# Performance work log

Measured on AMD Instinct MI355X. Metric: run time of the kernel, lower is better.

## Reference

```python
import jax, jax.numpy as jnp
import numpy as np

RADIUS = 0.5
HEADS = 4
LATENT = 128
KIN = 3 + 3 + 3 + 1  # q_pos + o_pos + rel + dist
LN_EPS = 1e-5


def setup_inputs() -> dict:
    key = jax.random.key(0)
    ks = jax.random.split(key, 12)
    B, Nq, No = 2, 1024, 1024
    h_obs = jax.random.normal(ks[0], (B, No, LATENT), dtype=jnp.float32)
    pos_obs = jax.random.uniform(ks[1], (B, No, 3), dtype=jnp.float32)
    pos_query = jax.random.uniform(ks[2], (B, Nq, 3), dtype=jnp.float32)
    obs_mask = jax.random.randint(ks[3], (B, No), 0, 2, dtype=jnp.int32)
    # kernel MLP params: Linear(KIN, LATENT) -> ReLU -> Linear(LATENT, HEADS)
    W1 = jax.random.normal(ks[4], (KIN, LATENT), dtype=jnp.float32) * (1.0 / np.sqrt(KIN))
    b1 = jax.random.normal(ks[5], (LATENT,), dtype=jnp.float32) * 0.01
    W2 = jax.random.normal(ks[6], (LATENT, HEADS), dtype=jnp.float32) * (1.0 / np.sqrt(LATENT))
    b2 = jax.random.normal(ks[7], (HEADS,), dtype=jnp.float32) * 0.01
    ln_g = jnp.ones((LATENT,), dtype=jnp.float32)
    ln_b = jnp.zeros((LATENT,), dtype=jnp.float32)
    Wv = jax.random.normal(ks[8], (LATENT, LATENT), dtype=jnp.float32) * (1.0 / np.sqrt(LATENT))
    bv = jax.random.normal(ks[9], (LATENT,), dtype=jnp.float32) * 0.01
    return {"h_obs": h_obs, "pos_obs": pos_obs, "pos_query": pos_query,
            "obs_mask": obs_mask, "W1": W1, "b1": b1, "W2": W2, "b2": b2,
            "ln_g": ln_g, "ln_b": ln_b, "Wv": Wv, "bv": bv}


def reference(h_obs, pos_obs, pos_query, obs_mask, W1, b1, W2, b2, ln_g, ln_b, Wv, bv):
    B, Nq, _ = pos_query.shape
    _, No, _ = pos_obs.shape
    H, D = HEADS, LATENT // HEADS

    # pairwise geometric encoding: (B, Nq, No, *)
    rel = pos_query[:, :, None, :] - pos_obs[:, None, :, :]
    dist = jnp.linalg.norm(rel, axis=-1, keepdims=True)
    q_exp = jnp.broadcast_to(pos_query[:, :, None, :], rel.shape)
    o_exp = jnp.broadcast_to(pos_obs[:, None, :, :], rel.shape)
    kin = jnp.concatenate([q_exp, o_exp, rel, dist], axis=-1)  # (B,Nq,No,KIN)

    # per-pair MLP -> per-head attention logits
    hid = jax.nn.relu(kin @ W1 + b1)                 # (B,Nq,No,LATENT)
    logits = hid @ W2 + b2                           # (B,Nq,No,H)
    logits = jnp.transpose(logits, (0, 3, 1, 2))     # (B,H,Nq,No)

    # radius + observation masking
    neg = jnp.float32(-jnp.inf)
    mask = (dist[..., 0] > RADIUS)[:, None, :, :] | (obs_mask == 0)[:, None, None, :]
    logits = jnp.where(mask, neg, logits)
    weights = jax.nn.softmax(logits, axis=-1)        # (B,H,Nq,No)

    # value path: LayerNorm + projection
    mu = jnp.mean(h_obs, axis=-1, keepdims=True)
    var = jnp.var(h_obs, axis=-1, keepdims=True)
    hn = (h_obs - mu) / jnp.sqrt(var + LN_EPS) * ln_g + ln_b
    v = hn @ Wv + bv                                 # (B,No,LATENT)
    v = jnp.transpose(v.reshape(B, No, H, D), (0, 2, 1, 3))  # (B,H,No,D)

    out = jnp.einsum('bhqo,bhod->bhqd', weights, v)  # (B,H,Nq,D)
    out = jnp.transpose(out, (0, 2, 1, 3)).reshape(B, Nq, H * D)
    return out
```

## Files before the change

kernel.cpp:

```cpp
#include <hip/hip_runtime.h>
#include <math.h>
#include <float.h>

#define B_ 2
#define NQ 1024
#define NO 1024
#define LAT 128
#define NHEADS 4
#define RADIUS_ 0.5f
#define LN_EPS_ 1e-5f
#define PW_STRIDE 68

#define V_BYTES ((size_t)B_ * NO * LAT * 4)

__device__ __forceinline__ float selh(int h, float a, float b, float c, float d) {
  return h == 0 ? a : (h == 1 ? b : (h == 2 ? c : d));
}

__global__ __launch_bounds__(256) void gano_prep_kernel(
    const float* __restrict__ h_obs, const float* __restrict__ ln_g,
    const float* __restrict__ ln_b, const float* __restrict__ Wv,
    const float* __restrict__ bv, float* __restrict__ v_out)
{
  const int tid = threadIdx.x;
  const int j = tid & 127;
  const int half = tid >> 7;
  const int wave = tid >> 6;
  const int lane = tid & 63;
  const int r0 = blockIdx.x * 4 + half * 2;

  __shared__ float s_redA[2][4];
  __shared__ float s_redB[2][4];
  __shared__ __align__(16) float s_hn[4][LAT];

  const float x0 = h_obs[(size_t)r0 * LAT + j];
  const float x1 = h_obs[(size_t)(r0 + 1) * LAT + j];
  float s0 = x0, s1 = x1;
  #pragma unroll
  for (int off = 32; off >= 1; off >>= 1) {
    s0 += __shfl_down(s0, off);
    s1 += __shfl_down(s1, off);
  }
  if (lane == 0) { s_redA[0][wave] = s0; s_redA[1][wave] = s1; }
  __syncthreads();
  const float mu0 = (s_redA[0][half * 2] + s_redA[0][half * 2 + 1]) * (1.0f / LAT);
  const float mu1 = (s_redA[1][half * 2] + s_redA[1][half * 2 + 1]) * (1.0f / LAT);
  const float d0 = x0 - mu0, d1 = x1 - mu1;
  float q0 = d0 * d0, q1 = d1 * d1;
  #pragma unroll
  for (int off = 32; off >= 1; off >>= 1) {
    q0 += __shfl_down(q0, off);
    q1 += __shfl_down(q1, off);
  }
  if (lane == 0) { s_redB[0][wave] = q0; s_redB[1][wave] = q1; }
  __syncthreads();
  const float var0 = (s_redB[0][half * 2] + s_redB[0][half * 2 + 1]) * (1.0f / LAT);
  const float var1 = (s_redB[1][half * 2] + s_redB[1][half * 2 + 1]) * (1.0f / LAT);
  const float g = ln_g[j], be = ln_b[j];
  s_hn[half * 2 + 0][j] = d0 * rsqrtf(var0 + LN_EPS_) * g + be;
  s_hn[half * 2 + 1][j] = d1 * rsqrtf(var1 + LN_EPS_) * g + be;
  __syncthreads();

  float a0 = 0.0f, a1 = 0.0f;
  const float4* h0 = (const float4*)s_hn[half * 2 + 0];
  const float4* h1 = (const float4*)s_hn[half * 2 + 1];
  #pragma unroll 4
  for (int k4 = 0; k4 < LAT / 4; ++k4) {
    const float4 u0 = h0[k4];
    const float4 u1 = h1[k4];
    const float w0 = Wv[(k4 * 4 + 0) * LAT + j];
    const float w1 = Wv[(k4 * 4 + 1) * LAT + j];
    const float w2 = Wv[(k4 * 4 + 2) * LAT + j];
    const float w3 = Wv[(k4 * 4 + 3) * LAT + j];
    a0 = fmaf(u0.x, w0, a0); a0 = fmaf(u0.y, w1, a0);
    a0 = fmaf(u0.z, w2, a0); a0 = fmaf(u0.w, w3, a0);
    a1 = fmaf(u1.x, w0, a1); a1 = fmaf(u1.y, w1, a1);
    a1 = fmaf(u1.z, w2, a1); a1 = fmaf(u1.w, w3, a1);
  }
  const float bvj = bv[j];
  v_out[(size_t)(r0 + 0) * LAT + j] = a0 + bvj;
  v_out[(size_t)(r0 + 1) * LAT + j] = a1 + bvj;
}

__global__ __launch_bounds__(256, 6) void gano_main_kernel(
    const float* __restrict__ pos_obs, const float* __restrict__ pos_query,
    const int* __restrict__ obs_mask,
    const float* __restrict__ W1, const float* __restrict__ b1,
    const float* __restrict__ W2, const float* __restrict__ b2,
    const float* __restrict__ v, float* __restrict__ out)
{
  __shared__ int   s_vidx[NO];
  __shared__ float s_vdist[NO];
  __shared__ __align__(16) float s_w[LAT][8];
  __shared__ __align__(16) float s_Q[LAT];
  __shared__ __align__(16) float s_pw[4][NHEADS][PW_STRIDE];
  __shared__ float s_mz[4][2][NHEADS];
  __shared__ int   s_cnt[16];

  const int tid = threadIdx.x;
  const int wave = tid >> 6, lane = tid & 63;
  const int bid = blockIdx.x;
  const int b = bid >> 10, q = bid & (NQ - 1);

  const float qx = pos_query[((size_t)b * NQ + q) * 3 + 0];
  const float qy = pos_query[((size_t)b * NQ + q) * 3 + 1];
  const float qz = pos_query[((size_t)b * NQ + q) * 3 + 2];

  if (tid < LAT) {
    const int j = tid;
    float w[10];
    #pragma unroll
    for (int k = 0; k < 10; ++k) w[k] = W1[k * LAT + j];
    s_w[j][0] = w[3] - w[6];
    s_w[j][1] = w[4] - w[7];
    s_w[j][2] = w[5] - w[8];
    s_w[j][3] = w[9];
    const float4 w2r = *(const float4*)&W2[j * NHEADS];
    s_w[j][4] = w2r.x; s_w[j][5] = w2r.y; s_w[j][6] = w2r.z; s_w[j][7] = w2r.w;
    s_Q[j] = b1[j] + qx * (w[0] + w[6]) + qy * (w[1] + w[7]) + qz * (w[2] + w[8]);
  }

  const float* pob = pos_obs + (size_t)b * NO * 3;
  const int*   om  = obs_mask + (size_t)b * NO;
  float dists[4];
  unsigned long long bals[4];
  #pragma unroll
  for (int rd = 0; rd < 4; ++rd) {
    const int o = (rd << 8) + tid;
    const float ox = pob[o * 3 + 0], oy = pob[o * 3 + 1], oz = pob[o * 3 + 2];
    const float rx = qx - ox, ry = qy - oy, rz = qz - oz;
    const float dist = sqrtf(rx * rx + ry * ry + rz * rz);
    const int ok = (om[o] != 0) && (dist <= RADIUS_);
    const unsigned long long bal = __ballot(ok);
    if (lane == 0) s_cnt[(rd << 2) + wave] = __popcll(bal);
    bals[rd] = bal;
    dists[rd] = dist;
  }
  __syncthreads();
  int Nv = 0;
  #pragma unroll
  for (int k = 0; k < 16; ++k) Nv += s_cnt[k];
  #pragma unroll
  for (int rd = 0; rd < 4; ++rd) {
    const int slot = (rd << 2) + wave;
    int base = 0;
    for (int k = 0; k < slot; ++k) base += s_cnt[k];
    if ((bals[rd] >> lane) & 1ull) {
      const int pos = base + __popcll(bals[rd] & ((1ull << lane) - 1ull));
      s_vidx[pos] = (rd << 8) + tid;
      s_vdist[pos] = dists[rd];
    }
  }
  __syncthreads();

  const int c0 = lane << 1;
  const int hh = lane >> 4;
  const float* vbl = v + (size_t)b * NO * LAT + c0;
  const float b20 = b2[0], b21 = b2[1], b22 = b2[2], b23 = b2[3];

  float m0 = -FLT_MAX, m1 = -FLT_MAX, m2 = -FLT_MAX, m3 = -FLT_MAX;
  float z0 = 0.f, z1 = 0.f, z2 = 0.f, z3 = 0.f;
  float ax = 0.f, ay = 0.f;

  for (int cbase = wave << 6; cbase < Nv; cbase += 256) {
    const int cnt = min(64, Nv - cbase);
    const bool act = lane < cnt;
    const int slot = cbase + (act ? lane : (cnt - 1));
    const int idx = s_vidx[slot];
    const float dist = s_vdist[slot];
    const float ox = pob[idx * 3 + 0], oy = pob[idx * 3 + 1], oz = pob[idx * 3 + 2];

    float a0 = b20, a1 = b21, a2 = b22, a3 = b23;
    #pragma unroll 2
    for (int j4 = 0; j4 < LAT / 4; ++j4) {
      const float4 q4 = *(const float4*)&s_Q[j4 << 2];
      #pragma unroll
      for (int u = 0; u < 4; ++u) {
        const int j = (j4 << 2) + u;
        const float4 cw = *(const float4*)&s_w[j][0];
        const float4 w2 = *(const float4*)&s_w[j][4];
        const float qj = (u == 0) ? q4.x : (u == 1) ? q4.y : (u == 2) ? q4.z : q4.w;
        float gg = fmaf(cw.x, ox, qj);
        gg = fmaf(cw.y, oy, gg);
        gg = fmaf(cw.z, oz, gg);
        gg = fmaf(cw.w, dist, gg);
        gg = fmaxf(gg, 0.0f);
        a0 = fmaf(gg, w2.x, a0);
        a1 = fmaf(gg, w2.y, a1);
        a2 = fmaf(gg, w2.z, a2);
        a3 = fmaf(gg, w2.w, a3);
      }
    }
    const float l0 = act ? a0 : -FLT_MAX;
    const float l1 = act ? a1 : -FLT_MAX;
    const float l2 = act ? a2 : -FLT_MAX;
    const float l3 = act ? a3 : -FLT_MAX;

    float x0 = l0, x1 = l1, x2 = l2, x3 = l3;
    #pragma unroll
    for (int off = 1; off < 64; off <<= 1) {
      x0 = fmaxf(x0, __shfl_xor(x0, off));
      x1 = fmaxf(x1, __shfl_xor(x1, off));
      x2 = fmaxf(x2, __shfl_xor(x2, off));
      x3 = fmaxf(x3, __shfl_xor(x3, off));
    }
    const float nm0 = fmaxf(m0, x0), nm1 = fmaxf(m1, x1);
    const float nm2 = fmaxf(m2, x2), nm3 = fmaxf(m3, x3);
    const float sc0 = __expf(m0 - nm0), sc1 = __expf(m1 - nm1);
    const float sc2 = __expf(m2 - nm2), sc3 = __expf(m3 - nm3);
    m0 = nm0; m1 = nm1; m2 = nm2; m3 = nm3;

    const float p0 = __expf(l0 - nm0);
    const float p1 = __expf(l1 - nm1);
    const float p2 = __expf(l2 - nm2);
    const float p3 = __expf(l3 - nm3);
    s_pw[wave][0][lane] = p0;
    s_pw[wave][1][lane] = p1;
    s_pw[wave][2][lane] = p2;
    s_pw[wave][3][lane] = p3;
    z0 = z0 * sc0 + p0;
    z1 = z1 * sc1 + p1;
    z2 = z2 * sc2 + p2;
    z3 = z3 * sc3 + p3;
    const float sch = selh(hh, sc0, sc1, sc2, sc3);
    ax *= sch; ay *= sch;

    const float* pr = s_pw[wave][hh];
    for (int it = 0; it < cnt; it += 4) {
      const float4 pq = *(const float4*)&pr[it];
      const int4 iq = *(const int4*)&s_vidx[cbase + it];
      const int i0 = iq.x & (NO - 1), i1 = iq.y & (NO - 1);
      const int i2 = iq.z & (NO - 1), i3 = iq.w & (NO - 1);
      const float2 v0 = *(const float2*)(vbl + (size_t)i0 * LAT);
      const float2 v1 = *(const float2*)(vbl + (size_t)i1 * LAT);
      const float2 v2 = *(const float2*)(vbl + (size_t)i2 * LAT);
      const float2 v3 = *(const float2*)(vbl + (size_t)i3 * LAT);
      ax = fmaf(pq.x, v0.x, ax); ay = fmaf(pq.x, v0.y, ay);
      ax = fmaf(pq.y, v1.x, ax); ay = fmaf(pq.y, v1.y, ay);
      ax = fmaf(pq.z, v2.x, ax); ay = fmaf(pq.z, v2.y, ay);
      ax = fmaf(pq.w, v3.x, ax); ay = fmaf(pq.w, v3.y, ay);
    }
  }

  #pragma unroll
  for (int off = 1; off < 64; off <<= 1) {
    z0 += __shfl_xor(z0, off);
    z1 += __shfl_xor(z1, off);
    z2 += __shfl_xor(z2, off);
    z3 += __shfl_xor(z3, off);
  }
  if (lane == 0) {
    s_mz[wave][0][0] = m0; s_mz[wave][0][1] = m1;
    s_mz[wave][0][2] = m2; s_mz[wave][0][3] = m3;
    s_mz[wave][1][0] = z0; s_mz[wave][1][1] = z1;
    s_mz[wave][1][2] = z2; s_mz[wave][1][3] = z3;
  }
  float* part = &s_pw[wave][0][0];
  part[c0] = ax; part[c0 + 1] = ay;
  __syncthreads();

  if (tid < LAT) {
    const int h = tid >> 5;
    const float mw0 = s_mz[0][0][h], mw1 = s_mz[1][0][h];
    const float mw2 = s_mz[2][0][h], mw3 = s_mz[3][0][h];
    const float M = fmaxf(fmaxf(mw0, mw1), fmaxf(mw2, mw3));
    float num = 0.f, den = 0.f;
    #pragma unroll
    for (int w = 0; w < 4; ++w) {
      const float e = __expf(s_mz[w][0][h] - M);
      num = fmaf(e, (&s_pw[w][0][0])[tid], num);
      den = fmaf(e, s_mz[w][1][h], den);
    }
    const float r = (Nv > 0) ? (num / den) : 0.0f;
    out[((size_t)b * NQ + q) * LAT + tid] = r;
  }
}

extern "C" void kernel_launch(void* const* d_in, const int* in_sizes, int n_in,
                              void* d_out, int out_size, void* d_ws, size_t ws_size,
                              hipStream_t stream) {
  const float* h_obs     = (const float*)d_in[0];
  const float* pos_obs   = (const float*)d_in[1];
  const float* pos_query = (const float*)d_in[2];
  const int*   obs_mask  = (const int*)d_in[3];
  const float* W1        = (const float*)d_in[4];
  const float* b1        = (const float*)d_in[5];
  const float* W2        = (const float*)d_in[6];
  const float* b2        = (const float*)d_in[7];
  const float* ln_g      = (const float*)d_in[8];
  const float* ln_b      = (const float*)d_in[9];
  const float* Wv        = (const float*)d_in[10];
  const float* bv        = (const float*)d_in[11];
  float* outp = (float*)d_out;
  float* v    = (float*)d_ws;

  gano_prep_kernel<<<(B_ * NO) / 4, 256, 0, stream>>>(h_obs, ln_g, ln_b, Wv, bv, v);
  gano_main_kernel<<<B_ * NQ, 256, 0, stream>>>(pos_obs, pos_query, obs_mask,
                                                W1, b1, W2, b2, v, outp);
}
```

Baseline: 47.13 us.

## Map one query per wave with streaming compaction and multi-slot flash passes

Each wave now owns one query instead of a whole block sharing one query. Within the wave, valid neighbours are compacted into a per-wave LDS list in chunks of up to 256 and processed with register-blocked online softmax over 1-4 slots per lane. Every __syncthreads and the cross-wave softmax merge are removed. Derived MLP weights (the folded W1 combinations and W2) are precomputed once by the prep kernel into workspace and read from global or cache instead of being rebuilt per block. In exchange, each query's MLP and value gather run on a single wave, raising register pressure and making load balance depend on neighbour counts.

Result: faster. 44.59 us (-5.4%).

```diff
diff --git a/kernel.cpp b/kernel.cpp
--- a/kernel.cpp
+++ b/kernel.cpp
@@ -9,18 +9,23 @@
 #define NHEADS 4
 #define RADIUS_ 0.5f
 #define LN_EPS_ 1e-5f
-#define PW_STRIDE 68
+#define CAP 256
+#define PPAD 264
 
 #define V_BYTES ((size_t)B_ * NO * LAT * 4)
 
 __device__ __forceinline__ float selh(int h, float a, float b, float c, float d) {
   return h == 0 ? a : (h == 1 ? b : (h == 2 ? c : d));
 }
+
 
 __global__ __launch_bounds__(256) void gano_prep_kernel(
     const float* __restrict__ h_obs, const float* __restrict__ ln_g,
     const float* __restrict__ ln_b, const float* __restrict__ Wv,
-    const float* __restrict__ bv, float* __restrict__ v_out)
+    const float* __restrict__ bv, const float* __restrict__ W1,
+    const float* __restrict__ b1, const float* __restrict__ W2,
+    float* __restrict__ v_out,
+    float4* __restrict__ A4, float4* __restrict__ CW8, int write_derived)
 {
   const int tid = threadIdx.x;
   const int j = tid & 127;
@@ -80,200 +85,242 @@
   const float bvj = bv[j];
   v_out[(size_t)(r0 + 0) * LAT + j] = a0 + bvj;
   v_out[(size_t)(r0 + 1) * LAT + j] = a1 + bvj;
-}
-
-__global__ __launch_bounds__(256, 6) void gano_main_kernel(
+
+  if (write_derived && blockIdx.x == 0 && tid < LAT) {
+    float w[10];
+    #pragma unroll
+    for (int k = 0; k < 10; ++k) w[k] = W1[k * LAT + tid];
+    A4[tid] = make_float4(w[0] + w[6], w[1] + w[7], w[2] + w[8], b1[tid]);
+    CW8[2 * tid + 0] = make_float4(w[3] - w[6], w[4] - w[7], w[5] - w[8], w[9]);
+    CW8[2 * tid + 1] = make_float4(W2[tid * NHEADS + 0], W2[tid * NHEADS + 1],
+                                   W2[tid * NHEADS + 2], W2[tid * NHEADS + 3]);
+  }
+}
+
+template <int NS, bool DERIVED>
+__device__ __forceinline__ void flash_pass(
+    int lane, int cnt,
+    const float4* __restrict__ s_list_w, const int* __restrict__ s_idx_w,
+    const float* __restrict__ s_Qw, float* __restrict__ s_pw,
+    const float4* __restrict__ CW8,
+    const float* __restrict__ W1, const float* __restrict__ W2,
+    float b20, float b21, float b22, float b23,
+    const float* __restrict__ vb, int hh,
+    float& m0, float& m1, float& m2, float& m3,
+    float& z0, float& z1, float& z2, float& z3,
+    float& ax, float& ay)
+{
+  float4 C[NS];
+  bool act[NS];
+  #pragma unroll
+  for (int r = 0; r < NS; ++r) {
+    const int s = r * 64 + lane;
+    act[r] = s < cnt;
+    C[r] = s_list_w[act[r] ? s : (cnt - 1)];
+  }
+  float L[NS][NHEADS];
+  #pragma unroll
+  for (int r = 0; r < NS; ++r) {
+    L[r][0] = b20; L[r][1] = b21; L[r][2] = b22; L[r][3] = b23;
+  }
+
+  #pragma unroll 2
+  for (int j4 = 0; j4 < LAT / 4; ++j4) {
+    const float4 q4 = *(const float4*)&s_Qw[j4 << 2];
+    #pragma unroll
+    for (int u = 0; u < 4; ++u) {
+      const int j = (j4 << 2) + u;
+      float4 cw, w2;
+      if constexpr (DERIVED) {
+        cw = CW8[2 * j + 0];
+        w2 = CW8[2 * j + 1];
+      } else {
+        cw = make_float4(W1[3 * LAT + j] - W1[6 * LAT + j],
+                         W1[4 * LAT + j] - W1[7 * LAT + j],
+                         W1[5 * LAT + j] - W1[8 * LAT + j],
+                         W1[9 * LAT + j]);
+        w2 = *(const float4*)&W2[j * NHEADS];
+      }
+      const float qj = (u == 0) ? q4.x : (u == 1) ? q4.y : (u == 2) ? q4.z : q4.w;
+      #pragma unroll
+      for (int r = 0; r < NS; ++r) {
+        float gg = fmaf(cw.x, C[r].x, qj);
+        gg = fmaf(cw.y, C[r].y, gg);
+        gg = fmaf(cw.z, C[r].z, gg);
+        gg = fmaf(cw.w, C[r].w, gg);
+        gg = fmaxf(gg, 0.0f);
+        L[r][0] = fmaf(gg, w2.x, L[r][0]);
+        L[r][1] = fmaf(gg, w2.y, L[r][1]);
+        L[r][2] = fmaf(gg, w2.z, L[r][2]);
+        L[r][3] = fmaf(gg, w2.w, L[r][3]);
+      }
+    }
+  }
+  #pragma unroll
+  for (int r = 0; r < NS; ++r)
+    if (!act[r]) { L[r][0] = L[r][1] = L[r][2] = L[r][3] = -FLT_MAX; }
+
+  float x0 = L[0][0], x1 = L[0][1], x2 = L[0][2], x3 = L[0][3];
+  #pragma unroll
+  for (int r = 1; r < NS; ++r) {
+    x0 = fmaxf(x0, L[r][0]); x1 = fmaxf(x1, L[r][1]);
+    x2 = fmaxf(x2, L[r][2]); x3 = fmaxf(x3, L[r][3]);
+  }
+  #pragma unroll
+  for (int off = 1; off < 64; off <<= 1) {
+    x0 = fmaxf(x0, __shfl_xor(x0, off));
+    x1 = fmaxf(x1, __shfl_xor(x1, off));
+    x2 = fmaxf(x2, __shfl_xor(x2, off));
+    x3 = fmaxf(x3, __shfl_xor(x3, off));
+  }
+  const float nm0 = fmaxf(m0, x0), nm1 = fmaxf(m1, x1);
+  const float nm2 = fmaxf(m2, x2), nm3 = fmaxf(m3, x3);
+  const float sc0 = __expf(m0 - nm0), sc1 = __expf(m1 - nm1);
+  const float sc2 = __expf(m2 - nm2), sc3 = __expf(m3 - nm3);
+  m0 = nm0; m1 = nm1; m2 = nm2; m3 = nm3;
+
+  float pz0 = 0.f, pz1 = 0.f, pz2 = 0.f, pz3 = 0.f;
+  #pragma unroll
+  for (int r = 0; r < NS; ++r) {
+    const float p0 = __expf(L[r][0] - nm0);
+    const float p1 = __expf(L[r][1] - nm1);
+    const float p2 = __expf(L[r][2] - nm2);
+    const float p3 = __expf(L[r][3] - nm3);
+    const int s = r * 64 + lane;
+    s_pw[0 * PPAD + s] = p0;
+    s_pw[1 * PPAD + s] = p1;
+    s_pw[2 * PPAD + s] = p2;
+    s_pw[3 * PPAD + s] = p3;
+    pz0 += p0; pz1 += p1; pz2 += p2; pz3 += p3;
+  }
+  #pragma unroll
+  for (int off = 1; off < 64; off <<= 1) {
+    pz0 += __shfl_xor(pz0, off);
+    pz1 += __shfl_xor(pz1, off);
+    pz2 += __shfl_xor(pz2, off);
+    pz3 += __shfl_xor(pz3, off);
+  }
+  z0 = z0 * sc0 + pz0;
+  z1 = z1 * sc1 + pz1;
+  z2 = z2 * sc2 + pz2;
+  z3 = z3 * sc3 + pz3;
+
+  const float sch = selh(hh, sc0, sc1, sc2, sc3);
+  ax *= sch; ay *= sch;
+  const float* pr = s_pw + hh * PPAD;
+  #pragma unroll 2
+  for (int it = 0; it < cnt; it += 4) {
+    const float4 pq = *(const float4*)&pr[it];
+    const int4 iq = *(const int4*)&s_idx_w[it];
+    const float2 v0 = *(const float2*)(vb + (size_t)(iq.x & (NO - 1)) * LAT);
+    const float2 v1 = *(const float2*)(vb + (size_t)(iq.y & (NO - 1)) * LAT);
+    const float2 v2 = *(const float2*)(vb + (size_t)(iq.z & (NO - 1)) * LAT);
+    const float2 v3 = *(const float2*)(vb + (size_t)(iq.w & (NO - 1)) * LAT);
+    ax = fmaf(pq.x, v0.x, ax); ay = fmaf(pq.x, v0.y, ay);
+    ax = fmaf(pq.y, v1.x, ax); ay = fmaf(pq.y, v1.y, ay);
+    ax = fmaf(pq.z, v2.x, ax); ay = fmaf(pq.z, v2.y, ay);
+    ax = fmaf(pq.w, v3.x, ax); ay = fmaf(pq.w, v3.y, ay);
+  }
+}
+
+template <bool DERIVED>
+__global__ __launch_bounds__(256, 4) void gano_main_kernel(
     const float* __restrict__ pos_obs, const float* __restrict__ pos_query,
     const int* __restrict__ obs_mask,
     const float* __restrict__ W1, const float* __restrict__ b1,
     const float* __restrict__ W2, const float* __restrict__ b2,
-    const float* __restrict__ v, float* __restrict__ out)
+    const float* __restrict__ v,
+    const float4* __restrict__ A4, const float4* __restrict__ CW8,
+    float* __restrict__ out)
 {
-  __shared__ int   s_vidx[NO];
-  __shared__ float s_vdist[NO];
-  __shared__ __align__(16) float s_w[LAT][8];
-  __shared__ __align__(16) float s_Q[LAT];
-  __shared__ __align__(16) float s_pw[4][NHEADS][PW_STRIDE];
-  __shared__ float s_mz[4][2][NHEADS];
-  __shared__ int   s_cnt[16];
+  __shared__ __align__(16) float4 s_list[4][CAP];
+  __shared__ int   s_idx[4][CAP];
+  __shared__ __align__(16) float s_p[4][NHEADS * PPAD];
+  __shared__ __align__(16) float s_Q[4][LAT];
 
   const int tid = threadIdx.x;
   const int wave = tid >> 6, lane = tid & 63;
-  const int bid = blockIdx.x;
-  const int b = bid >> 10, q = bid & (NQ - 1);
-
-  const float qx = pos_query[((size_t)b * NQ + q) * 3 + 0];
-  const float qy = pos_query[((size_t)b * NQ + q) * 3 + 1];
-  const float qz = pos_query[((size_t)b * NQ + q) * 3 + 2];
-
-  if (tid < LAT) {
-    const int j = tid;
-    float w[10];
-    #pragma unroll
-    for (int k = 0; k < 10; ++k) w[k] = W1[k * LAT + j];
-    s_w[j][0] = w[3] - w[6];
-    s_w[j][1] = w[4] - w[7];
-    s_w[j][2] = w[5] - w[8];
-    s_w[j][3] = w[9];
-    const float4 w2r = *(const float4*)&W2[j * NHEADS];
-    s_w[j][4] = w2r.x; s_w[j][5] = w2r.y; s_w[j][6] = w2r.z; s_w[j][7] = w2r.w;
-    s_Q[j] = b1[j] + qx * (w[0] + w[6]) + qy * (w[1] + w[7]) + qz * (w[2] + w[8]);
+  const int qg = blockIdx.x * 4 + wave;
+  const int b = qg >> 10, q = qg & (NQ - 1);
+
+  const float qx = pos_query[(size_t)qg * 3 + 0];
+  const float qy = pos_query[(size_t)qg * 3 + 1];
+  const float qz = pos_query[(size_t)qg * 3 + 2];
+
+  #pragma unroll
+  for (int jj = lane; jj < LAT; jj += 64) {
+    float4 a;
+    if constexpr (DERIVED) {
+      a = A4[jj];
+    } else {
+      a = make_float4(W1[0 * LAT + jj] + W1[6 * LAT + jj],
+                      W1[1 * LAT + jj] + W1[7 * LAT + jj],
+                      W1[2 * LAT + jj] + W1[8 * LAT + jj],
+                      b1[jj]);
+    }
+    s_Q[wave][jj] = fmaf(qx, a.x, fmaf(qy, a.y, fmaf(qz, a.z, a.w)));
   }
 
   const float* pob = pos_obs + (size_t)b * NO * 3;
   const int*   om  = obs_mask + (size_t)b * NO;
-  float dists[4];
-  unsigned long long bals[4];
-  #pragma unroll
-  for (int rd = 0; rd < 4; ++rd) {
-    const int o = (rd << 8) + tid;
+  const float b20 = b2[0], b21 = b2[1], b22 = b2[2], b23 = b2[3];
+  const int c0 = lane << 1;
+  const int hh = lane >> 4;
+  const float* vb = v + (size_t)b * NO * LAT + c0;
+
+  float m0 = -FLT_MAX, m1 = -FLT_MAX, m2 = -FLT_MAX, m3 = -FLT_MAX;
+  float z0 = 0.f, z1 = 0.f, z2 = 0.f, z3 = 0.f;
+  float ax = 0.f, ay = 0.f;
+
+  const float4* listw = s_list[wave];
+  const int*    idxw  = s_idx[wave];
+  const float*  Qw    = s_Q[wave];
+  float*        pw    = s_p[wave];
+
+  int base = 0, nvtot = 0;
+
+  #define RUN_PASS(N_)                                                        \
+    flash_pass<N_, DERIVED>(lane, base, listw, idxw, Qw, pw, CW8, W1, W2,     \
+                            b20, b21, b22, b23, vb, hh,                        \
+                            m0, m1, m2, m3, z0, z1, z2, z3, ax, ay)
+  #define DISPATCH_PASS()                                                     \
+    do {                                                                      \
+      const int ns_ = (base + 63) >> 6;                                       \
+      if (ns_ == 4)      RUN_PASS(4);                                         \
+      else if (ns_ == 3) RUN_PASS(3);                                         \
+      else if (ns_ == 2) RUN_PASS(2);                                         \
+      else               RUN_PASS(1);                                         \
+    } while (0)
+
+  for (int rd = 0; rd < 16; ++rd) {
+    const int o = (rd << 6) + lane;
     const float ox = pob[o * 3 + 0], oy = pob[o * 3 + 1], oz = pob[o * 3 + 2];
     const float rx = qx - ox, ry = qy - oy, rz = qz - oz;
     const float dist = sqrtf(rx * rx + ry * ry + rz * rz);
     const int ok = (om[o] != 0) && (dist <= RADIUS_);
     const unsigned long long bal = __ballot(ok);
-    if (lane == 0) s_cnt[(rd << 2) + wave] = __popcll(bal);
-    bals[rd] = bal;
-    dists[rd] = dist;
-  }
-  __syncthreads();
-  int Nv = 0;
-  #pragma unroll
-  for (int k = 0; k < 16; ++k) Nv += s_cnt[k];
-  #pragma unroll
-  for (int rd = 0; rd < 4; ++rd) {
-    const int slot = (rd << 2) + wave;
-    int base = 0;
-    for (int k = 0; k < slot; ++k) base += s_cnt[k];
-    if ((bals[rd] >> lane) & 1ull) {
-      const int pos = base + __popcll(bals[rd] & ((1ull << lane) - 1ull));
-      s_vidx[pos] = (rd << 8) + tid;
-      s_vdist[pos] = dists[rd];
+    const int cnt = __popcll(bal);
+    if (base + cnt > CAP) {
+      DISPATCH_PASS();
+      base = 0;
     }
-  }
-  __syncthreads();
-
-  const int c0 = lane << 1;
-  const int hh = lane >> 4;
-  const float* vbl = v + (size_t)b * NO * LAT + c0;
-  const float b20 = b2[0], b21 = b2[1], b22 = b2[2], b23 = b2[3];
-
-  float m0 = -FLT_MAX, m1 = -FLT_MAX, m2 = -FLT_MAX, m3 = -FLT_MAX;
-  float z0 = 0.f, z1 = 0.f, z2 = 0.f, z3 = 0.f;
-  float ax = 0.f, ay = 0.f;
-
-  for (int cbase = wave << 6; cbase < Nv; cbase += 256) {
-    const int cnt = min(64, Nv - cbase);
-    const bool act = lane < cnt;
-    const int slot = cbase + (act ? lane : (cnt - 1));
-    const int idx = s_vidx[slot];
-    const float dist = s_vdist[slot];
-    const float ox = pob[idx * 3 + 0], oy = pob[idx * 3 + 1], oz = pob[idx * 3 + 2];
-
-    float a0 = b20, a1 = b21, a2 = b22, a3 = b23;
-    #pragma unroll 2
-    for (int j4 = 0; j4 < LAT / 4; ++j4) {
-      const float4 q4 = *(const float4*)&s_Q[j4 << 2];
-      #pragma unroll
-      for (int u = 0; u < 4; ++u) {
-        const int j = (j4 << 2) + u;
-        const float4 cw = *(const float4*)&s_w[j][0];
-        const float4 w2 = *(const float4*)&s_w[j][4];
-        const float qj = (u == 0) ? q4.x : (u == 1) ? q4.y : (u == 2) ? q4.z : q4.w;
-        float gg = fmaf(cw.x, ox, qj);
-        gg = fmaf(cw.y, oy, gg);
-        gg = fmaf(cw.z, oz, gg);
-        gg = fmaf(cw.w, dist, gg);
-        gg = fmaxf(gg, 0.0f);
-        a0 = fmaf(gg, w2.x, a0);
-        a1 = fmaf(gg, w2.y, a1);
-        a2 = fmaf(gg, w2.z, a2);
-        a3 = fmaf(gg, w2.w, a3);
-      }
+    if (ok) {
+      const int pos = base + __popcll(bal & ((1ull << lane) - 1ull));
+      s_list[wave][pos] = make_float4(ox, oy, oz, dist);
+      s_idx[wave][pos] = o;
     }
-    const float l0 = act ? a0 : -FLT_MAX;
-    const float l1 = act ? a1 : -FLT_MAX;
-    const float l2 = act ? a2 : -FLT_MAX;
-    const float l3 = act ? a3 : -FLT_MAX;
-
-    float x0 = l0, x1 = l1, x2 = l2, x3 = l3;
-    #pragma unroll
-    for (int off = 1; off < 64; off <<= 1) {
-      x0 = fmaxf(x0, __shfl_xor(x0, off));
-      x1 = fmaxf(x1, __shfl_xor(x1, off));
-      x2 = fmaxf(x2, __shfl_xor(x2, off));
-      x3 = fmaxf(x3, __shfl_xor(x3, off));
-    }
-    const float nm0 = fmaxf(m0, x0), nm1 = fmaxf(m1, x1);
-    const float nm2 = fmaxf(m2, x2), nm3 = fmaxf(m3, x3);
-    const float sc0 = __expf(m0 - nm0), sc1 = __expf(m1 - nm1);
-    const float sc2 = __expf(m2 - nm2), sc3 = __expf(m3 - nm3);
-    m0 = nm0; m1 = nm1; m2 = nm2; m3 = nm3;
-
-    const float p0 = __expf(l0 - nm0);
-    const float p1 = __expf(l1 - nm1);
-    const float p2 = __expf(l2 - nm2);
-    const float p3 = __expf(l3 - nm3);
-    s_pw[wave][0][lane] = p0;
-    s_pw[wave][1][lane] = p1;
-    s_pw[wave][2][lane] = p2;
-    s_pw[wave][3][lane] = p3;
-    z0 = z0 * sc0 + p0;
-    z1 = z1 * sc1 + p1;
-    z2 = z2 * sc2 + p2;
-    z3 = z3 * sc3 + p3;
-    const float sch = selh(hh, sc0, sc1, sc2, sc3);
-    ax *= sch; ay *= sch;
-
-    const float* pr = s_pw[wave][hh];
-    for (int it = 0; it < cnt; it += 4) {
-      const float4 pq = *(const float4*)&pr[it];
-      const int4 iq = *(const int4*)&s_vidx[cbase + it];
-      const int i0 = iq.x & (NO - 1), i1 = iq.y & (NO - 1);
-      const int i2 = iq.z & (NO - 1), i3 = iq.w & (NO - 1);
-      const float2 v0 = *(const float2*)(vbl + (size_t)i0 * LAT);
-      const float2 v1 = *(const float2*)(vbl + (size_t)i1 * LAT);
-      const float2 v2 = *(const float2*)(vbl + (size_t)i2 * LAT);
-      const float2 v3 = *(const float2*)(vbl + (size_t)i3 * LAT);
-      ax = fmaf(pq.x, v0.x, ax); ay = fmaf(pq.x, v0.y, ay);
-      ax = fmaf(pq.y, v1.x, ax); ay = fmaf(pq.y, v1.y, ay);
-      ax = fmaf(pq.z, v2.x, ax); ay = fmaf(pq.z, v2.y, ay);
-      ax = fmaf(pq.w, v3.x, ax); ay = fmaf(pq.w, v3.y, ay);
-    }
-  }
-
-  #pragma unroll
-  for (int off = 1; off < 64; off <<= 1) {
-    z0 += __shfl_xor(z0, off);
-    z1 += __shfl_xor(z1, off);
-    z2 += __shfl_xor(z2, off);
-    z3 += __shfl_xor(z3, off);
-  }
-  if (lane == 0) {
-    s_mz[wave][0][0] = m0; s_mz[wave][0][1] = m1;
-    s_mz[wave][0][2] = m2; s_mz[wave][0][3] = m3;
-    s_mz[wave][1][0] = z0; s_mz[wave][1][1] = z1;
-    s_mz[wave][1][2] = z2; s_mz[wave][1][3] = z3;
-  }
-  float* part = &s_pw[wave][0][0];
-  part[c0] = ax; part[c0 + 1] = ay;
-  __syncthreads();
-
-  if (tid < LAT) {
-    const int h = tid >> 5;
-    const float mw0 = s_mz[0][0][h], mw1 = s_mz[1][0][h];
-    const float mw2 = s_mz[2][0][h], mw3 = s_mz[3][0][h];
-    const float M = fmaxf(fmaxf(mw0, mw1), fmaxf(mw2, mw3));
-    float num = 0.f, den = 0.f;
-    #pragma unroll
-    for (int w = 0; w < 4; ++w) {
-      const float e = __expf(s_mz[w][0][h] - M);
-      num = fmaf(e, (&s_pw[w][0][0])[tid], num);
-      den = fmaf(e, s_mz[w][1][h], den);
-    }
-    const float r = (Nv > 0) ? (num / den) : 0.0f;
-    out[((size_t)b * NQ + q) * LAT + tid] = r;
-  }
+    base += cnt;
+    nvtot += cnt;
+  }
+  if (base > 0) DISPATCH_PASS();
+  #undef RUN_PASS
+  #undef DISPATCH_PASS
+
+  const float zz = selh(hh, z0, z1, z2, z3);
+  float2 o2;
+  o2.x = (nvtot > 0) ? (ax / zz) : 0.0f;
+  o2.y = (nvtot > 0) ? (ay / zz) : 0.0f;
+  *(float2*)&out[(size_t)qg * LAT + c0] = o2;
 }
 
 extern "C" void kernel_launch(void* const* d_in, const int* in_sizes, int n_in,
@@ -294,7 +341,21 @@
   float* outp = (float*)d_out;
   float* v    = (float*)d_ws;
 
-  gano_prep_kernel<<<(B_ * NO) / 4, 256, 0, stream>>>(h_obs, ln_g, ln_b, Wv, bv, v);
-  gano_main_kernel<<<B_ * NQ, 256, 0, stream>>>(pos_obs, pos_query, obs_mask,
-                                                W1, b1, W2, b2, v, outp);
-}
+  const size_t need = V_BYTES + 3 * LAT * sizeof(float4);
+  const int derived = (ws_size >= need) ? 1 : 0;
+  float4* A4  = (float4*)((char*)d_ws + V_BYTES);
+  float4* CW8 = A4 + LAT;
+  if (!derived) { A4 = (float4*)d_ws; CW8 = (float4*)d_ws; }
+
+  gano_prep_kernel<<<(B_ * NO) / 4, 256, 0, stream>>>(h_obs, ln_g, ln_b, Wv, bv,
+                                                      W1, b1, W2, v, A4, CW8, derived);
+  if (derived) {
+    gano_main_kernel<true><<<(B_ * NQ) / 4, 256, 0, stream>>>(
+        pos_obs, pos_query, obs_mask, W1, b1, W2, b2, v,
+        (const float4*)A4, (const float4*)CW8, outp);
+  } else {
+    gano_main_kernel<false><<<(B_ * NQ) / 4, 256, 0, stream>>>(
+        pos_obs, pos_query, obs_mask, W1, b1, W2, b2, v,
+        (const float4*)A4, (const float4*)CW8, outp);
+  }
+}
```
